# Kernel optimization log

Measured on AMD Instinct MI355X. Metric: run time of the kernel, lower is better.

Reference implementation:

```python
import jax, jax.numpy as jnp
import numpy as np

B, TAPE, N, F = 128, 100000, 50000, 32

def setup_inputs() -> dict:
    key = jax.random.key(0)
    k1, k2, k3, k4 = jax.random.split(key, 4)
    tape = jax.random.normal(k1, (B, TAPE), dtype=jnp.float32)
    input_indices = jax.random.randint(k2, (N, F), 0, TAPE)
    # He init scaled by fan-in, padding slots (index==0) zeroed as in __init__
    weights = jax.random.normal(k3, (N, F), dtype=jnp.float32) * jnp.sqrt(2.0 / F)
    weights = jnp.where(input_indices == 0, 0.0, weights)
    bias = jnp.zeros((N,), dtype=jnp.float32)
    output_indices = jnp.arange(N)
    act_type = jax.random.randint(k4, (N,), 0, 2)
    return {"tape": tape, "weights": weights, "bias": bias,
            "input_indices": input_indices, "output_indices": output_indices,
            "act_type": act_type}

def reference(tape, weights, bias, input_indices, output_indices, act_type):
    # gather padded fan-in inputs: [B, N, F]
    gathered = tape[:, input_indices]
    # weighted sum over fan-in + bias: [B, N]
    x = jnp.einsum('bnf,nf->bn', gathered, weights) + bias
    # per-activation-type apply (two activation groups: relu / tanh)
    x = jnp.where(act_type == 0, jax.nn.relu(x), jnp.tanh(x))
    # scatter results back into tape
    return tape.at[:, output_indices].set(x)
```

## Files before the change

kernel.cpp:

```cpp
#include <hip/hip_runtime.h>
#include <cmath>

#define TAPE_SZ 100000
#define N_SZ    50000
#define F_SZ    32
#define B_SZ    128
#define GSUB    32
#define NGRP    4
#define HSPLIT  50000
#define NBV     64
#define NCHUNK  ((N_SZ + NBV - 1) / NBV)
#define GRID_G  ((NCHUNK / 2) * 8)

static __device__ __forceinline__ unsigned short f32_to_bf16(float f) {
    unsigned int u = __float_as_uint(f);
    u = (u + 0x7fffu + ((u >> 16) & 1u)) >> 16;
    return (unsigned short)u;
}

__global__ __launch_bounds__(256) void transpose_g32(const float* __restrict__ in,
                                                     unsigned short* __restrict__ outG,
                                                     float* __restrict__ out) {
    __shared__ float tile[32][129];
    const int x0 = blockIdx.x * 32;
    const int tx = threadIdx.x;
    const int ty = threadIdx.y;

    #pragma unroll
    for (int yy = ty; yy < B_SZ; yy += 8)
        tile[tx][yy] = in[(size_t)yy * TAPE_SZ + x0 + tx];
    __syncthreads();

    const int tid = ty * 32 + tx;
    const int l = tid >> 3;
    const int o = tid & 7;
    const int g = o >> 1;
    const int hf = o & 1;
    unsigned short* dst = outG + ((size_t)g * TAPE_SZ + x0 + l) * GSUB + hf * 16;
    union { unsigned short u[8]; uint4 q; } p0, p1;
    #pragma unroll
    for (int k = 0; k < 8; ++k) {
        p0.u[k] = f32_to_bf16(tile[l][g * GSUB + hf * 16 + k]);
        p1.u[k] = f32_to_bf16(tile[l][g * GSUB + hf * 16 + 8 + k]);
    }
    *(uint4*)dst       = p0.q;
    *(uint4*)(dst + 8) = p1.q;

    if (x0 + tx >= N_SZ) {
        #pragma unroll
        for (int yy = ty; yy < B_SZ; yy += 8)
            out[(size_t)yy * TAPE_SZ + x0 + tx] = tile[tx][yy];
    }
}

template<int HALF>
__global__ __launch_bounds__(256) void gather_h(
    const unsigned short* __restrict__ tapeG,
    const float* __restrict__ weights,
    const float* __restrict__ bias,
    const int*   __restrict__ in_idx,
    const int*   __restrict__ out_idx,
    const int*   __restrict__ act_type,
    float* __restrict__ acc,
    float* __restrict__ out) {
    __shared__ union {
        int2  iw[NBV][33];
        float x[GSUB][66];
    } u;
    __shared__ float s_bias[NBV];
    __shared__ int   s_act[NBV];
    __shared__ int   s_oidx[NBV];

    const int tid   = threadIdx.x;
    const int i     = blockIdx.x;
    const int g     = i & 3;
    const int sub   = (i >> 2) & 1;
    const int chunk = (i >> 3) * 2 + sub;
    const int n0    = chunk * NBV;
    const int nend  = min(NBV, N_SZ - n0);

    for (int t = tid; t < nend * 32; t += 256) {
        const int n = t >> 5, f = t & 31;
        u.iw[n][f] = make_int2(in_idx[(size_t)n0 * 32 + t],
                               __float_as_int(weights[(size_t)n0 * 32 + t]));
    }
    if (HALF == 1 && tid < nend) {
        s_bias[tid] = bias[n0 + tid];
        s_act[tid]  = act_type[n0 + tid];
        s_oidx[tid] = out_idx[n0 + tid];
    }
    __syncthreads();

    const int nl  = tid >> 2;
    const int seg = tid & 3;
    const bool an = (nl < nend);
    const unsigned short* tg = tapeG + (size_t)g * TAPE_SZ * GSUB + seg * 8;

    float a[8];
    #pragma unroll
    for (int k = 0; k < 8; ++k) a[k] = 0.f;

    #pragma unroll
    for (int fo = 0; fo < 32; fo += 8) {
        int r8[8]; float w8[8];
        #pragma unroll
        for (int j = 0; j < 8; ++j) {
            const int2 iw = u.iw[nl][fo + j];
            r8[j] = iw.x; w8[j] = __int_as_float(iw.y);
        }
        uint4 q8[8];
        #pragma unroll
        for (int j = 0; j < 8; ++j) {
            q8[j] = make_uint4(0u, 0u, 0u, 0u);
            const bool c = an && (HALF == 0 ? (r8[j] < HSPLIT) : (r8[j] >= HSPLIT));
            if (c) q8[j] = *(const uint4*)(tg + (size_t)r8[j] * GSUB);
        }
        #pragma unroll
        for (int j = 0; j < 8; ++j) {
            const float wv = w8[j];
            a[0] = fmaf(__uint_as_float(q8[j].x << 16),         wv, a[0]);
            a[1] = fmaf(__uint_as_float(q8[j].x & 0xffff0000u), wv, a[1]);
            a[2] = fmaf(__uint_as_float(q8[j].y << 16),         wv, a[2]);
            a[3] = fmaf(__uint_as_float(q8[j].y & 0xffff0000u), wv, a[3]);
            a[4] = fmaf(__uint_as_float(q8[j].z << 16),         wv, a[4]);
            a[5] = fmaf(__uint_as_float(q8[j].z & 0xffff0000u), wv, a[5]);
            a[6] = fmaf(__uint_as_float(q8[j].w << 16),         wv, a[6]);
            a[7] = fmaf(__uint_as_float(q8[j].w & 0xffff0000u), wv, a[7]);
        }
    }

    float* ap = acc + (size_t)(n0 + nl) * B_SZ + g * GSUB + seg * 8;
    if (HALF == 0) {
        if (an) {
            *(float4*)(ap)     = make_float4(a[0], a[1], a[2], a[3]);
            *(float4*)(ap + 4) = make_float4(a[4], a[5], a[6], a[7]);
        }
        return;
    }

    if (an) {
        const float4 p0 = *(const float4*)(ap);
        const float4 p1 = *(const float4*)(ap + 4);
        a[0] += p0.x; a[1] += p0.y; a[2] += p0.z; a[3] += p0.w;
        a[4] += p1.x; a[5] += p1.y; a[6] += p1.z; a[7] += p1.w;
        const float bz = s_bias[nl];
        const int   at = s_act[nl];
        #pragma unroll
        for (int k = 0; k < 8; ++k) {
            const float v = a[k] + bz;
            a[k] = (at == 0) ? fmaxf(v, 0.f) : tanhf(v);
        }
    }
    __syncthreads();
    if (an) {
        #pragma unroll
        for (int k = 0; k < 8; ++k) u.x[seg * 8 + k][nl] = a[k];
    }
    __syncthreads();

    const int quads = (nend + 3) >> 2;
    for (int it = tid; it < GSUB * quads; it += 256) {
        int bl, j4;
        if (nend == NBV) { bl = it >> 4; j4 = it & 15; }
        else             { bl = it / quads; j4 = it - bl * quads; }
        const int nq  = j4 * 4;
        const int oc0 = s_oidx[nq];
        float* orow = out + (size_t)(g * GSUB + bl) * TAPE_SZ;
        const bool consec = (nq + 3 < nend) &&
                            (s_oidx[nq + 1] == oc0 + 1) &&
                            (s_oidx[nq + 2] == oc0 + 2) &&
                            (s_oidx[nq + 3] == oc0 + 3) && ((oc0 & 3) == 0);
        if (consec) {
            *(float4*)(orow + oc0) = make_float4(u.x[bl][nq + 0], u.x[bl][nq + 1],
                                                 u.x[bl][nq + 2], u.x[bl][nq + 3]);
        } else {
            #pragma unroll
            for (int c = 0; c < 4; ++c)
                if (nq + c < nend) orow[s_oidx[nq + c]] = u.x[bl][nq + c];
        }
    }
}

__global__ __launch_bounds__(128) void gather_fallback(const float* __restrict__ tape,
                                                       const float* __restrict__ weights,
                                                       const float* __restrict__ bias,
                                                       const int*   __restrict__ in_idx,
                                                       const int*   __restrict__ out_idx,
                                                       const int*   __restrict__ act_type,
                                                       float* __restrict__ out) {
    const int n = blockIdx.x;
    const int b = threadIdx.x;
    float acc = 0.f;
    for (int f = 0; f < F_SZ; ++f) {
        acc += tape[(size_t)b * TAPE_SZ + in_idx[(size_t)n * F_SZ + f]] *
               weights[(size_t)n * F_SZ + f];
    }
    acc += bias[n];
    acc = (act_type[n] == 0) ? fmaxf(acc, 0.f) : tanhf(acc);
    out[(size_t)b * TAPE_SZ + out_idx[n]] = acc;
}

__global__ __launch_bounds__(256) void copy_tail_fb(const float* __restrict__ tape,
                                                    float* __restrict__ out) {
    const int n4 = (TAPE_SZ - N_SZ) / 4;
    int i = blockIdx.x * blockDim.x + threadIdx.x;
    int b = blockIdx.y;
    if (i < n4) {
        const float4* src = (const float4*)(tape + (size_t)b * TAPE_SZ + N_SZ);
        float4*       dst = (float4*)(out  + (size_t)b * TAPE_SZ + N_SZ);
        dst[i] = src[i];
    }
}

extern "C" void kernel_launch(void* const* d_in, const int* in_sizes, int n_in,
                              void* d_out, int out_size, void* d_ws, size_t ws_size,
                              hipStream_t stream) {
    const float* tape    = (const float*)d_in[0];
    const float* weights = (const float*)d_in[1];
    const float* bias    = (const float*)d_in[2];
    const int*   in_idx  = (const int*)d_in[3];
    const int*   out_idx = (const int*)d_in[4];
    const int*   act     = (const int*)d_in[5];
    float*       out     = (float*)d_out;

    const size_t one = (size_t)TAPE_SZ * B_SZ * sizeof(unsigned short);
    if (ws_size >= 2 * one) {
        unsigned short* tapeG = (unsigned short*)d_ws;
        float*          accp  = (float*)((char*)d_ws + one);
        transpose_g32<<<dim3(TAPE_SZ / 32), dim3(32, 8), 0, stream>>>(tape, tapeG, out);
        gather_h<0><<<dim3(GRID_G), dim3(256), 0, stream>>>(
            tapeG, weights, bias, in_idx, out_idx, act, accp, out);
        gather_h<1><<<dim3(GRID_G), dim3(256), 0, stream>>>(
            tapeG, weights, bias, in_idx, out_idx, act, accp, out);
    } else {
        copy_tail_fb<<<dim3(((TAPE_SZ - N_SZ) / 4 + 255) / 256, B_SZ), 256, 0, stream>>>(tape, out);
        gather_fallback<<<dim3(N_SZ), 128, 0, stream>>>(
            tape, weights, bias, in_idx, out_idx, act, out);
    }
}
```

Before: 204.4 us.

## Merge split-range two-pass gather into a single full-range gather kernel

```diff
diff --git a/kernel.cpp b/kernel.cpp
--- a/kernel.cpp
+++ b/kernel.cpp
@@ -7,10 +7,9 @@
 #define B_SZ    128
 #define GSUB    32
 #define NGRP    4
-#define HSPLIT  50000
 #define NBV     64
 #define NCHUNK  ((N_SZ + NBV - 1) / NBV)
-#define GRID_G  ((NCHUNK / 2) * 8)
+#define GRID_G  (NCHUNK * NGRP)
 
 static __device__ __forceinline__ unsigned short f32_to_bf16(float f) {
     unsigned int u = __float_as_uint(f);
@@ -53,15 +52,13 @@
     }
 }
 
-template<int HALF>
-__global__ __launch_bounds__(256) void gather_h(
+__global__ __launch_bounds__(256) void gather_full(
     const unsigned short* __restrict__ tapeG,
     const float* __restrict__ weights,
     const float* __restrict__ bias,
     const int*   __restrict__ in_idx,
     const int*   __restrict__ out_idx,
     const int*   __restrict__ act_type,
-    float* __restrict__ acc,
     float* __restrict__ out) {
     __shared__ union {
         int2  iw[NBV][33];
@@ -72,10 +69,8 @@
     __shared__ int   s_oidx[NBV];
 
     const int tid   = threadIdx.x;
-    const int i     = blockIdx.x;
-    const int g     = i & 3;
-    const int sub   = (i >> 2) & 1;
-    const int chunk = (i >> 3) * 2 + sub;
+    const int g     = blockIdx.x & 3;
+    const int chunk = blockIdx.x >> 2;
     const int n0    = chunk * NBV;
     const int nend  = min(NBV, N_SZ - n0);
 
@@ -84,7 +79,7 @@
         u.iw[n][f] = make_int2(in_idx[(size_t)n0 * 32 + t],
                                __float_as_int(weights[(size_t)n0 * 32 + t]));
     }
-    if (HALF == 1 && tid < nend) {
+    if (tid < nend) {
         s_bias[tid] = bias[n0 + tid];
         s_act[tid]  = act_type[n0 + tid];
         s_oidx[tid] = out_idx[n0 + tid];
@@ -112,8 +107,7 @@
         #pragma unroll
         for (int j = 0; j < 8; ++j) {
             q8[j] = make_uint4(0u, 0u, 0u, 0u);
-            const bool c = an && (HALF == 0 ? (r8[j] < HSPLIT) : (r8[j] >= HSPLIT));
-            if (c) q8[j] = *(const uint4*)(tg + (size_t)r8[j] * GSUB);
+            if (an) q8[j] = *(const uint4*)(tg + (size_t)r8[j] * GSUB);
         }
         #pragma unroll
         for (int j = 0; j < 8; ++j) {
@@ -129,20 +123,7 @@
         }
     }
 
-    float* ap = acc + (size_t)(n0 + nl) * B_SZ + g * GSUB + seg * 8;
-    if (HALF == 0) {
-        if (an) {
-            *(float4*)(ap)     = make_float4(a[0], a[1], a[2], a[3]);
-            *(float4*)(ap + 4) = make_float4(a[4], a[5], a[6], a[7]);
-        }
-        return;
-    }
-
     if (an) {
-        const float4 p0 = *(const float4*)(ap);
-        const float4 p1 = *(const float4*)(ap + 4);
-        a[0] += p0.x; a[1] += p0.y; a[2] += p0.z; a[3] += p0.w;
-        a[4] += p1.x; a[5] += p1.y; a[6] += p1.z; a[7] += p1.w;
         const float bz = s_bias[nl];
         const int   at = s_act[nl];
         #pragma unroll
@@ -223,15 +204,12 @@
     const int*   act     = (const int*)d_in[5];
     float*       out     = (float*)d_out;
 
-    const size_t one = (size_t)TAPE_SZ * B_SZ * sizeof(unsigned short);
-    if (ws_size >= 2 * one) {
+    const size_t need = (size_t)TAPE_SZ * B_SZ * sizeof(unsigned short);
+    if (ws_size >= need) {
         unsigned short* tapeG = (unsigned short*)d_ws;
-        float*          accp  = (float*)((char*)d_ws + one);
         transpose_g32<<<dim3(TAPE_SZ / 32), dim3(32, 8), 0, stream>>>(tape, tapeG, out);
-        gather_h<0><<<dim3(GRID_G), dim3(256), 0, stream>>>(
-            tapeG, weights, bias, in_idx, out_idx, act, accp, out);
-        gather_h<1><<<dim3(GRID_G), dim3(256), 0, stream>>>(
-            tapeG, weights, bias, in_idx, out_idx, act, accp, out);
+        gather_full<<<dim3(GRID_G), dim3(256), 0, stream>>>(
+            tapeG, weights, bias, in_idx, out_idx, act, out);
     } else {
         copy_tail_fb<<<dim3(((TAPE_SZ - N_SZ) / 4 + 255) / 256, B_SZ), 256, 0, stream>>>(tape, out);
         gather_fallback<<<dim3(N_SZ), 128, 0, stream>>>(
```

Result: faster. 187.6 us (-8.2%).
